# Performance work log

Measured on AMD Instinct MI355X. Metric: run time of the kernel, lower is better.

## Reference

```python
import jax, jax.numpy as jnp
import numpy as np

# --- model dims (from init_kwargs + Mamba3 args) ---
D_MODEL = 256            # hidden_dim
D_INNER = 2 * D_MODEL    # expand=2
D_STATE = 8
HEADDIM = 16
NHEADS = D_INNER // HEADDIM  # 32
CHUNK = 8
D_CONV = 4
CONV_DIM = D_INNER + 2 * D_STATE            # x,B,C share the depthwise conv
D_INPROJ = 2 * D_INNER + 2 * D_STATE + NHEADS  # z,xBC,dt
INPUT_DIM = 57
OUT_SIZE = 6
BATCH = 16
SEQLEN = 4096


def setup_inputs() -> dict:
    key = jax.random.key(0)
    ks = jax.random.split(key, 12)
    def w(k, shape, s=0.02):
        return jax.random.normal(k, shape, dtype=jnp.float32) * s
    # dt bias initialized so softplus(dt_bias) ~ [1e-3, 1e-1] (Mamba-style)
    dt0 = jnp.exp(jax.random.uniform(ks[4], (NHEADS,), minval=jnp.log(1e-3), maxval=jnp.log(1e-1)))
    dt_bias = dt0 + jnp.log(-jnp.expm1(-dt0))  # inverse softplus
    return {
        "x": jax.random.normal(ks[0], (BATCH, SEQLEN, INPUT_DIM), dtype=jnp.float32),
        "W_in": w(ks[1], (D_MODEL, INPUT_DIM)),
        "b_in": jnp.zeros((D_MODEL,), jnp.float32),
        "W_inproj": w(ks[2], (D_INPROJ, D_MODEL)),
        "conv_w": w(ks[3], (CONV_DIM, D_CONV), 0.2),
        "conv_b": jnp.zeros((CONV_DIM,), jnp.float32),
        "dt_bias": dt_bias.astype(jnp.float32),
        "A_log": jnp.log(jax.random.uniform(ks[5], (NHEADS,), minval=1.0, maxval=16.0)).astype(jnp.float32),
        "D": jnp.ones((NHEADS,), jnp.float32),
        "W_out": w(ks[6], (D_MODEL, D_INNER)),
        "W_cls": w(ks[7], (OUT_SIZE, D_MODEL)),
        "b_cls": jnp.zeros((OUT_SIZE,), jnp.float32),
    }


def reference(x, W_in, b_in, W_inproj, conv_w, conv_b, dt_bias, A_log, D, W_out, W_cls, b_cls):
    Bsz, Lq, _ = x.shape
    h = x @ W_in.T + b_in                                  # [B,L,D_MODEL]
    zxbcdt = h @ W_inproj.T                                # [B,L,D_INPROJ]
    z = zxbcdt[..., :D_INNER]
    xBC = zxbcdt[..., D_INNER:D_INNER + CONV_DIM]
    dt = zxbcdt[..., -NHEADS:]
    # causal depthwise conv1d (kernel D_CONV) + SiLU
    xp = jnp.pad(xBC, ((0, 0), (D_CONV - 1, 0), (0, 0)))
    conv = sum(xp[:, k:k + Lq, :] * conv_w[:, k] for k in range(D_CONV)) + conv_b
    xBC = jax.nn.silu(conv)
    xs = xBC[..., :D_INNER]
    Bm = xBC[..., D_INNER:D_INNER + D_STATE]               # [B,L,N]
    Cm = xBC[..., -D_STATE:]                               # [B,L,N]
    dt = jax.nn.softplus(dt + dt_bias)                     # [B,L,H]
    A = -jnp.exp(A_log)                                    # [H]
    # --- chunked SSD selective scan (SISO: scalar A per head) ---
    Nc = Lq // CHUNK
    xh = xs.reshape(Bsz, Nc, CHUNK, NHEADS, HEADDIM)
    Bc = Bm.reshape(Bsz, Nc, CHUNK, D_STATE)
    Cc = Cm.reshape(Bsz, Nc, CHUNK, D_STATE)
    dtc = dt.reshape(Bsz, Nc, CHUNK, NHEADS)
    cA = jnp.cumsum(dtc * A, axis=2)                       # [B,Nc,cs,H]
    # intra-chunk: y_i += sum_{j<=i} (C_i.B_j) exp(cA_i-cA_j) dt_j x_j
    Lmat = jnp.exp(cA[:, :, :, None, :] - cA[:, :, None, :, :])   # [B,Nc,i,j,H]
    mask = jnp.tril(jnp.ones((CHUNK, CHUNK), bool))
    Lmat = jnp.where(mask[None, None, :, :, None], Lmat, 0.0)
    CB = jnp.einsum('bcin,bcjn->bcij', Cc, Bc)
    scores = CB[..., None] * Lmat * dtc[:, :, None, :, :]
    y_intra = jnp.einsum('bcijh,bcjhp->bcihp', scores, xh)
    # per-chunk end states and decays
    dec_end = jnp.exp(cA[:, :, -1:, :] - cA)               # [B,Nc,cs,H]
    S = jnp.einsum('bcjh,bcjn,bcjhp->bchpn', dec_end * dtc, Bc, xh)
    chunk_dec = jnp.exp(cA[:, :, -1, :])                   # [B,Nc,H]
    def step(hc, inp):
        Sc, dc = inp
        return hc * dc[:, :, None, None] + Sc, hc          # emit state BEFORE chunk
    h0 = jnp.zeros((Bsz, NHEADS, HEADDIM, D_STATE), x.dtype)
    _, hprev = jax.lax.scan(step, h0, (jnp.moveaxis(S, 1, 0), jnp.moveaxis(chunk_dec, 1, 0)))
    hprev = jnp.moveaxis(hprev, 0, 1)                      # [B,Nc,H,P,N]
    y_inter = jnp.einsum('bchpn,bcin,bcih->bcihp', hprev, Cc, jnp.exp(cA))
    y = y_intra + y_inter + D[None, None, None, :, None] * xh
    y = y.reshape(Bsz, Lq, D_INNER)
    y = y * jax.nn.silu(z)                                 # z gate (no out-proj norm)
    out = y @ W_out.T                                      # [B,L,D_MODEL]
    pooled = out.mean(axis=1)                              # AdaptiveAvgPool1d(1)
    return pooled @ W_cls.T + b_cls                        # [B,OUT_SIZE]
```

## Files before the change

kernel.cpp:

```cpp
#include <hip/hip_runtime.h>
#include <math.h>

#define BATCH 16
#define SEQLEN 4096
#define INPUT_DIM 57
#define D_MODEL 256
#define D_INNER 512
#define D_STATE 8
#define HEADDIM 16
#define NHEADS 32
#define CHUNK 8
#define NC (SEQLEN/CHUNK)
#define NCH (NC/2)
#define CONV_DIM 528
#define D_INPROJ 1072
#define OUT_SIZE 6
#define NTOK (BATCH*SEQLEN)
#define NSEG 16
#define SEGC (NCH/NSEG)

__device__ __forceinline__ unsigned short f2bf(float f) {
    unsigned v = __float_as_uint(f);
    return (unsigned short)((v + 0x7fffu + ((v >> 16) & 1u)) >> 16);
}
__device__ __forceinline__ unsigned pack_bf2(float lo, float hi) {
    unsigned r;
    asm("v_cvt_pk_bf16_f32 %0, %1, %2" : "=v"(r) : "v"(lo), "v"(hi));
    return r;
}
__device__ __forceinline__ float fsilu(float v) {
    return v * __builtin_amdgcn_rcpf(1.f + __expf(-v));
}

typedef __attribute__((ext_vector_type(8))) short bf16x8;
typedef __attribute__((ext_vector_type(4))) float f32x4;

__global__ __launch_bounds__(256) void precompute_kernel(
    const float* __restrict__ W_in,
    const float* __restrict__ b_in,
    const float* __restrict__ W_inproj,
    const float* __restrict__ W_out,
    const float* __restrict__ W_cls,
    float* __restrict__ WcT,
    float* __restrict__ b_comb,
    unsigned short* __restrict__ Wbf,
    float* __restrict__ W_oc)
{
    __shared__ double red[256];
    const int blk = blockIdx.x;
    const int tid = threadIdx.x;
    if (blk < D_INPROJ) {
        const int n = blk;
        const int t = tid & 63, ms = tid >> 6;
        double a0 = 0.0, a1 = 0.0;
        const int m0 = ms*64;
        if (t < INPUT_DIM) {
            for (int m = m0; m < m0 + 64; m += 2) {
                a0 += (double)W_inproj[n*D_MODEL+m  ] * (double)W_in[(m  )*INPUT_DIM+t];
                a1 += (double)W_inproj[n*D_MODEL+m+1] * (double)W_in[(m+1)*INPUT_DIM+t];
            }
        } else if (t == INPUT_DIM) {
            for (int m = m0; m < m0 + 64; m += 2) {
                a0 += (double)W_inproj[n*D_MODEL+m  ] * (double)b_in[m  ];
                a1 += (double)W_inproj[n*D_MODEL+m+1] * (double)b_in[m+1];
            }
        }
        red[tid] = a0 + a1;
        __syncthreads();
        if (tid < 64) {
            double acc = (red[tid] + red[tid+64]) + (red[tid+128] + red[tid+192]);
            if (t < INPUT_DIM) {
                WcT[t*D_INPROJ + n] = (float)acc;
                if (n < 1024) Wbf[n*64 + t] = f2bf((float)acc);
            } else {
                if (t == INPUT_DIM) b_comb[n] = (float)acc;
                if (n < 1024) Wbf[n*64 + t] = 0;
            }
        }
    } else {
        const int d = blk - D_INPROJ;
        const int o = tid >> 5;
        const int lp = tid & 31;
        double a = 0.0;
        if (o < OUT_SIZE) {
            const int m0 = lp*8;
            #pragma unroll
            for (int mm = 0; mm < 8; ++mm) {
                int m = m0 + mm;
                a += (double)W_cls[o*D_MODEL+m] * (double)W_out[m*D_INNER+d];
            }
        }
        #pragma unroll
        for (int off = 16; off > 0; off >>= 1)
            a += __shfl_down(a, off, 32);
        if (o < OUT_SIZE && lp == 0)
            W_oc[o*D_INNER + d] = (float)a;
    }
}

#define XS(r,k)       uni[(r)*68 + (k)]
#define EX(r,c)       uni[2176 + (r)*48 + (c)]
#define ELS2(cw,h,i)  uni[3088 + (((cw)*32+(h))*8) + (i)]
#define GCO2(cw,h,j)  uni[3600 + (((cw)*32+(h))*8) + (j)]
#define SCL3(cw,h,o)  uni[(((cw)*32+(h))*48) + (o)]

__global__ __launch_bounds__(256) void fused_kernel(
    const float* __restrict__ x,
    const unsigned short* __restrict__ Wbf,
    const float* __restrict__ WcT,
    const float* __restrict__ bcomb,
    const float* __restrict__ conv_w,
    const float* __restrict__ conv_b,
    const float* __restrict__ dt_bias,
    const float* __restrict__ A_log,
    const float* __restrict__ Dvec,
    unsigned* __restrict__ SGg,
    float* __restrict__ cdec,
    float* __restrict__ partial_intra)
{
    __shared__ __attribute__((aligned(16))) float uni[4112];
    __shared__ __attribute__((aligned(16))) float Bs[2][8][12], Cs[2][8][12];
    __shared__ float dts[2][8][33], cAl[2][8][33];
    __shared__ float CBl[2][8][8];

    const int blk = blockIdx.x;
    const int b = blk >> 8, cp = blk & 255;
    const int scBase = (b << 8) + cp;
    const int tid = threadIdx.x;
    const long t0 = (long)b*SEQLEN + (long)cp*16;
    const bool first = (cp == 0);

    #pragma unroll
    for (int it = 0; it < 8; ++it) {
        int idx = tid + it*256;
        int r = idx >> 6, k = idx & 63;
        float v = 0.f;
        if (k < INPUT_DIM && (r >= 16 || !first))
            v = x[(t0 - 16 + r)*INPUT_DIM + k];
        XS(r, k) = v;
    }
    __syncthreads();

    const int lane = tid & 63, wv = tid >> 6;
    const int quad = lane >> 4, mrow = lane & 15;

    bf16x8 aM[2], aH[2];
    #pragma unroll
    for (int hf = 0; hf < 2; ++hf) {
        const float* sm = &XS(16 + mrow, hf*32 + quad*8);
        const float* sh = &XS(mrow,      hf*32 + quad*8);
        unsigned* pm = (unsigned*)&aM[hf];
        unsigned* ph = (unsigned*)&aH[hf];
        #pragma unroll
        for (int j = 0; j < 4; ++j) {
            pm[j] = pack_bf2(sm[2*j], sm[2*j+1]);
            ph[j] = pack_bf2(sh[2*j], sh[2*j+1]);
        }
    }

    if (tid < 192) {
        const int col = tid % 48;
        const int grp = tid / 48;
        const int r0 = grp*5;
        const int nr = (grp == 3) ? 4 : 5;
        const float be = bcomb[1024 + col];
        float a[5];
        #pragma unroll
        for (int j = 0; j < 5; ++j) a[j] = be;
        for (int k = 0; k < INPUT_DIM; ++k) {
            const float w = WcT[(size_t)k*D_INPROJ + 1024 + col];
            #pragma unroll
            for (int j = 0; j < 5; ++j)
                if (j < nr) a[j] += w*XS(13 + r0 + j, k);
        }
        #pragma unroll
        for (int j = 0; j < 5; ++j) {
            if (j < nr) {
                int r = r0 + j;
                EX(r, col) = (first && r < 3) ? 0.f : a[j];
            }
        }
    }
    __syncthreads();

    if (tid < 32) {
        const int cw = tid >> 4, q = tid & 15;
        const int ch = 512 + q;
        const float4 cw4 = *(const float4*)&conv_w[ch*4];
        const float cb = conv_b[ch];
        float s0 = EX(cw*8+0, q), s1 = EX(cw*8+1, q), s2 = EX(cw*8+2, q);
        #pragma unroll
        for (int i = 0; i < 8; ++i) {
            float s3 = EX(cw*8+i+3, q);
            float v = cb + s0*cw4.x + s1*cw4.y + s2*cw4.z + s3*cw4.w;
            v = fsilu(v);
            if (q < 8) Bs[cw][i][q] = v; else Cs[cw][i][q-8] = v;
            s0 = s1; s1 = s2; s2 = s3;
        }
    } else if (tid >= 64 && tid < 128) {
        const int cw = (tid - 64) >> 5, h = (tid - 64) & 31;
        const float Ah = -__expf(A_log[h]);
        const float db = dt_bias[h];
        float ca = 0.f;
        #pragma unroll
        for (int i = 0; i < 8; ++i) {
            float raw = EX(cw*8 + i + 3, 16 + h) + db;
            float dt = (raw > 20.f) ? raw : log1pf(__expf(raw));
            dts[cw][i][h] = dt;
            ca += dt * Ah;
            cAl[cw][i][h] = ca;
            ELS2(cw, h, i) = __expf(ca);
        }
    }
    __syncthreads();

    if (tid < 128) {
        const int cw = tid >> 6, i = (tid >> 3) & 7, j = tid & 7;
        float s = 0.f;
        #pragma unroll
        for (int n = 0; n < 8; ++n) s += Cs[cw][i][n]*Bs[cw][j][n];
        CBl[cw][i][j] = s;
    } else if (tid < 160) {
        const int h = tid - 128;
        cdec[(size_t)scBase*32 + h] = ELS2(0, h, 7) * ELS2(1, h, 7);
    }
    __syncthreads();

    #pragma unroll
    for (int q = 0; q < 12; ++q) {
        int idx = tid + q*256;
        int ofs = idx % 48;
        int hc  = idx / 48;
        int h2 = hc & 31, cw2 = hc >> 5;
        int i, j;
        if (ofs < 16) { i = ofs >> 2; j = ofs & 3; }
        else { int r2 = ofs - 16; i = 4 + (r2 >> 3); j = r2 & 7; }
        float v = 0.f;
        if (j <= i)
            v = CBl[cw2][i][j]
              * __expf(cAl[cw2][i][h2] - cAl[cw2][j][h2]) * dts[cw2][j][h2];
        SCL3(cw2, h2, ofs) = v;
    }
    #pragma unroll
    for (int q = 0; q < 2; ++q) {
        int idx = tid + q*256;
        int j = idx & 7; int hc = idx >> 3;
        int h2 = hc & 31, cw2 = hc >> 5;
        GCO2(cw2, h2, j) = __expf(cAl[cw2][7][h2] - cAl[cw2][j][h2]) * dts[cw2][j][h2];
    }
    __syncthreads();

    const int cw   = quad >> 1;
    const int joff = (quad & 1) * 4;
    const int srcConv = (lane + 48) & 63;
    const float zm = (quad & 1) ? 0.f : 1.f;

    #pragma unroll
    for (int t = 0; t < 8; ++t) {
        const int g   = wv + 4*t;
        const int h   = g;
        const int col = g*16 + mrow;

        const unsigned short* wpz = &Wbf[(size_t)col*64];
        bf16x8 bz0 = *(const bf16x8*)&wpz[quad*8];
        bf16x8 bz1 = *(const bf16x8*)&wpz[32 + quad*8];
        const float bvz = bcomb[col];
        f32x4 accZ; accZ.x = bvz; accZ.y = bvz; accZ.z = bvz; accZ.w = bvz;
        accZ = __builtin_amdgcn_mfma_f32_16x16x32_bf16(aM[0], bz0, accZ, 0, 0, 0);
        accZ = __builtin_amdgcn_mfma_f32_16x16x32_bf16(aM[1], bz1, accZ, 0, 0, 0);

        const unsigned short* wpx = &Wbf[(size_t)(col + 512)*64];
        bf16x8 bx0 = *(const bf16x8*)&wpx[quad*8];
        bf16x8 bx1 = *(const bf16x8*)&wpx[32 + quad*8];
        const float bvx = bcomb[col + 512];
        f32x4 accXM; accXM.x = bvx; accXM.y = bvx; accXM.z = bvx; accXM.w = bvx;
        accXM = __builtin_amdgcn_mfma_f32_16x16x32_bf16(aM[0], bx0, accXM, 0, 0, 0);
        accXM = __builtin_amdgcn_mfma_f32_16x16x32_bf16(aM[1], bx1, accXM, 0, 0, 0);
        f32x4 accXH; accXH.x = bvx; accXH.y = bvx; accXH.z = bvx; accXH.w = bvx;
        accXH = __builtin_amdgcn_mfma_f32_16x16x32_bf16(aH[0], bx0, accXH, 0, 0, 0);
        accXH = __builtin_amdgcn_mfma_f32_16x16x32_bf16(aH[1], bx1, accXH, 0, 0, 0);

        float s1 = (quad == 3) ? accXH[3] : accXM[3];
        float s2 = (quad == 3) ? accXH[2] : accXM[2];
        float s3 = (quad == 3) ? accXH[1] : accXM[1];
        float r1 = __shfl(s1, srcConv, 64);
        float r2 = __shfl(s2, srcConv, 64);
        float r3 = __shfl(s3, srcConv, 64);
        if (first && quad == 0) { r1 = 0.f; r2 = 0.f; r3 = 0.f; }

        const float4 cw4 = *(const float4*)&conv_w[col*4];
        const float cb = conv_b[col];
        float vals[7] = {r3, r2, r1, accXM[0], accXM[1], accXM[2], accXM[3]};
        float xv[4], szv[4];
        #pragma unroll
        for (int r = 0; r < 4; ++r) {
            float v = cb + vals[r]*cw4.x + vals[r+1]*cw4.y + vals[r+2]*cw4.z + vals[r+3]*cw4.w;
            xv[r] = fsilu(v);
            szv[r] = fsilu(accZ[r]);
        }

        const float* sbase = &SCL3(cw, h, 0);
        float part[8];
        #pragma unroll
        for (int i = 0; i < 4; ++i) {
            f32x4 c4 = *(const f32x4*)&sbase[i*4];
            part[i] = zm*(c4[0]*xv[0] + c4[1]*xv[1] + c4[2]*xv[2] + c4[3]*xv[3]);
        }
        #pragma unroll
        for (int i = 4; i < 8; ++i) {
            f32x4 c4 = *(const f32x4*)&sbase[16 + (i-4)*8 + joff];
            part[i] = c4[0]*xv[0] + c4[1]*xv[1] + c4[2]*xv[2] + c4[3]*xv[3];
        }

        const float Dv = Dvec[h];
        float pa = 0.f;
        #pragma unroll
        for (int r = 0; r < 4; ++r) {
            float mine   = (quad & 1) ? part[4+r] : part[r];
            float theirs = (quad & 1) ? part[r]   : part[4+r];
            float other  = __shfl_xor(theirs, 16, 64);
            float y = Dv*xv[r] + mine + other;
            pa += y * szv[r];
        }
        pa += __shfl_xor(pa, 16, 64);
        float paO = __shfl_xor(pa, 32, 64);

        f32x4 G4 = *(const f32x4*)&GCO2(cw, h, joff);
        f32x4 E4 = *(const f32x4*)&ELS2(cw, h, joff);
        float sn[8], gg[8];
        #pragma unroll
        for (int n = 0; n < 8; ++n) { sn[n] = 0.f; gg[n] = 0.f; }
        #pragma unroll
        for (int r = 0; r < 4; ++r) {
            const int il = joff + r;
            float w  = szv[r]*E4[r];
            float uu = G4[r]*xv[r];
            const float4 B0 = *(const float4*)&Bs[cw][il][0];
            const float4 B1 = *(const float4*)&Bs[cw][il][4];
            const float4 C0 = *(const float4*)&Cs[cw][il][0];
            const float4 C1 = *(const float4*)&Cs[cw][il][4];
            sn[0] += uu*B0.x; sn[1] += uu*B0.y; sn[2] += uu*B0.z; sn[3] += uu*B0.w;
            sn[4] += uu*B1.x; sn[5] += uu*B1.y; sn[6] += uu*B1.z; sn[7] += uu*B1.w;
            gg[0] += w*C0.x;  gg[1] += w*C0.y;  gg[2] += w*C0.z;  gg[3] += w*C0.w;
            gg[4] += w*C1.x;  gg[5] += w*C1.y;  gg[6] += w*C1.z;  gg[7] += w*C1.w;
        }
        float sC[8], gC[8];
        #pragma unroll
        for (int n = 0; n < 8; ++n) {
            unsigned pk = pack_bf2(sn[n], gg[n]);
            unsigned pv = (unsigned)__shfl_xor((int)pk, 16, 64);
            sC[n] = sn[n] + __uint_as_float(pv << 16);
            gC[n] = gg[n] + __uint_as_float(pv & 0xffff0000u);
        }
        const float d0 = ELS2(0, h, 7), d1 = ELS2(1, h, 7);
        float local = 0.f;
        unsigned up[8];
        #pragma unroll
        for (int n = 0; n < 8; ++n) {
            unsigned pk = pack_bf2(sC[n], gC[n]);
            unsigned pv = (unsigned)__shfl_xor((int)pk, 32, 64);
            float So = __uint_as_float(pv << 16);
            float go = __uint_as_float(pv & 0xffff0000u);
            float Sp = sC[n]*d1 + So;
            float Gp = gC[n] + d0*go;
            local += sC[n]*go;
            up[n] = pack_bf2(Sp, Gp);
        }
        if (quad == 0) {
            partial_intra[(size_t)scBase*512 + col] = pa + paO + local;
            unsigned* dst = &SGg[((size_t)scBase*32 + h)*128 + mrow*8];
            *(uint4*)&dst[0] = *(uint4*)&up[0];
            *(uint4*)&dst[4] = *(uint4*)&up[4];
        }
    }
}

__global__ __launch_bounds__(128) void scanseg_kernel(
    const unsigned* __restrict__ SGg,
    const float* __restrict__ cdec,
    float* __restrict__ Sloc,
    float* __restrict__ Gseg,
    float* __restrict__ Aseg,
    float* __restrict__ ploc)
{
    const int blk = blockIdx.x;
    const int seg = blk & (NSEG-1);
    const int bh  = blk >> 4;
    const int b = bh >> 5, h = bh & 31;
    const int tid = threadIdx.x;
    const int c0 = seg*SEGC;

    float s = 0.f, P = 1.f, G = 0.f, pooled = 0.f;
    const unsigned* src = &SGg[((size_t)(b*NCH + c0)*32 + h)*128 + tid];
    const float* dsrc = &cdec[(b*NCH + c0)*32 + h];

    #pragma unroll 4
    for (int cc = 0; cc < SEGC; ++cc) {
        unsigned u = src[(size_t)cc*4096];
        float d = dsrc[cc*32];
        float Sv = __uint_as_float(u << 16);
        float gv = __uint_as_float(u & 0xffff0000u);
        pooled += s * gv;
        G += P * gv;
        P *= d;
        s = s*d + Sv;
    }
    Sloc[(size_t)blk*128 + tid] = s;
    Gseg[(size_t)blk*128 + tid] = G;
    if (tid == 0) Aseg[blk] = P;

    float t = pooled;
    t += __shfl_down(t, 4, 8);
    t += __shfl_down(t, 2, 8);
    t += __shfl_down(t, 1, 8);
    if ((tid & 7) == 0) ploc[(size_t)blk*16 + (tid >> 3)] = t;
}

__global__ __launch_bounds__(128) void scancomb_kernel(
    const float* __restrict__ Sloc,
    const float* __restrict__ Gseg,
    const float* __restrict__ Aseg,
    const float* __restrict__ ploc,
    double* __restrict__ partial_inter)
{
    __shared__ double red[128];
    const int bh = blockIdx.x;
    const int tid = threadIdx.x;
    float s = 0.f;
    double acc = 0.0;
    for (int seg = 0; seg < NSEG; ++seg) {
        size_t base = (size_t)(bh*NSEG + seg);
        float Gv = Gseg[base*128 + tid];
        float Av = Aseg[base];
        float Sv = Sloc[base*128 + tid];
        acc += (double)(s * Gv);
        s = s*Av + Sv;
    }
    red[tid] = acc;
    __syncthreads();
    if (tid < 16) {
        double t = 0.0;
        #pragma unroll
        for (int n = 0; n < 8; ++n) t += red[tid*8 + n];
        for (int seg = 0; seg < NSEG; ++seg)
            t += (double)ploc[(size_t)(bh*NSEG + seg)*16 + tid];
        partial_inter[(size_t)bh*16 + tid] = t;
    }
}

__global__ __launch_bounds__(256) void reduce_intra_kernel(
    const float* __restrict__ pIn,
    float* __restrict__ pred)
{
    const int g = blockIdx.x & 31;
    const int b = blockIdx.x >> 5;
    const int tid = threadIdx.x;
    for (int col = tid; col < 512; col += 256) {
        float s = 0.f;
        #pragma unroll 4
        for (int c = 0; c < 8; ++c)
            s += pIn[((size_t)b*NCH + g*8 + c)*512 + col];
        pred[((size_t)(b*32) + g)*512 + col] = s;
    }
}

__global__ __launch_bounds__(512) void final_kernel(
    const float* __restrict__ pred,
    const double* __restrict__ partial_inter,
    const float* __restrict__ W_oc,
    const float* __restrict__ b_cls,
    float* __restrict__ out)
{
    __shared__ double pooled[512];
    const int b = blockIdx.x, tid = threadIdx.x;
    double ssum = 0.0;
    for (int g = 0; g < 32; ++g)
        ssum += (double)pred[((size_t)(b*32) + g)*512 + tid];
    ssum += partial_inter[(size_t)b*512 + tid];
    pooled[tid] = ssum * (1.0/(double)SEQLEN);
    __syncthreads();
    if (tid < OUT_SIZE*64) {
        const int o = tid >> 6, l = tid & 63;
        double acc = 0.0;
        for (int m = l; m < 512; m += 64)
            acc += pooled[m] * (double)W_oc[o*512 + m];
        #pragma unroll
        for (int off = 32; off > 0; off >>= 1)
            acc += __shfl_down(acc, off);
        if (l == 0) out[b*OUT_SIZE + o] = (float)(acc + (double)b_cls[o]);
    }
}

extern "C" void kernel_launch(void* const* d_in, const int* in_sizes, int n_in,
                              void* d_out, int out_size, void* d_ws, size_t ws_size,
                              hipStream_t stream)
{
    const float* x        = (const float*)d_in[0];
    const float* W_in     = (const float*)d_in[1];
    const float* b_in     = (const float*)d_in[2];
    const float* W_inproj = (const float*)d_in[3];
    const float* conv_w   = (const float*)d_in[4];
    const float* conv_b   = (const float*)d_in[5];
    const float* dt_bias  = (const float*)d_in[6];
    const float* A_log    = (const float*)d_in[7];
    const float* Dvec     = (const float*)d_in[8];
    const float* W_out    = (const float*)d_in[9];
    const float* W_cls    = (const float*)d_in[10];
    const float* b_cls    = (const float*)d_in[11];
    float* out = (float*)d_out;

    char* ws = (char*)d_ws;
    size_t off = 0;
    auto alloc = [&](size_t bytes) -> void* {
        void* p = ws + off;
        off += (bytes + 255) & ~(size_t)255;
        return p;
    };
    unsigned* SGg = (unsigned*)alloc((size_t)BATCH*NCH*32*128*4);
    float*  cdecb = (float*) alloc((size_t)BATCH*NCH*32*4);
    float*  pIn   = (float*) alloc((size_t)BATCH*NCH*512*4);
    float*  SlocB = (float*) alloc((size_t)BATCH*NHEADS*NSEG*128*4);
    float*  GsegB = (float*) alloc((size_t)BATCH*NHEADS*NSEG*128*4);
    float*  AsegB = (float*) alloc((size_t)BATCH*NHEADS*NSEG*4);
    float*  plocB = (float*) alloc((size_t)BATCH*NHEADS*NSEG*16*4);
    float*  pred  = (float*) alloc((size_t)BATCH*32*512*4);
    double* pIt   = (double*)alloc((size_t)BATCH*512*8);
    float*  WcT   = (float*) alloc((size_t)INPUT_DIM*D_INPROJ*4);
    float*  bcomb = (float*) alloc((size_t)D_INPROJ*4);
    unsigned short* Wbf = (unsigned short*)alloc((size_t)1024*64*2);
    float*  Woc   = (float*) alloc((size_t)OUT_SIZE*D_INNER*4);
    if (off > ws_size) return;

    precompute_kernel<<<D_INPROJ + D_INNER, 256, 0, stream>>>(W_in, b_in, W_inproj, W_out, W_cls,
                                                              WcT, bcomb, Wbf, Woc);
    fused_kernel<<<BATCH*NC/2, 256, 0, stream>>>(x, Wbf, WcT, bcomb, conv_w, conv_b,
                                                 dt_bias, A_log, Dvec, SGg, cdecb, pIn);
    scanseg_kernel<<<BATCH*NHEADS*NSEG, 128, 0, stream>>>(SGg, cdecb, SlocB, GsegB, AsegB, plocB);
    scancomb_kernel<<<BATCH*NHEADS, 128, 0, stream>>>(SlocB, GsegB, AsegB, plocB, pIt);
    reduce_intra_kernel<<<BATCH*32, 256, 0, stream>>>(pIn, pred);
    final_kernel<<<BATCH, 512, 0, stream>>>(pred, pIt, Woc, b_cls, out);
}
```

Measured before the change: 293.2 us.

## Fuse intra-chunk reduction into fused kernel via atomics and consolidate shared memory

Removes the reduce_intra kernel and its pIn buffer: the fused kernel now atomically adds each per-chunk-pair partial sum straight into pred, which the precompute kernel zeroes beforehand. Shared memory is packed into one union array, B and C are merged into a single array, and the cumulative-A array is dropped. The exp of differences is replaced by a ratio of stored exponentials. This saves one launch and a global round trip, at the cost of atomic contention and some risk to accuracy from dividing exponentials.

```diff
diff --git a/kernel.cpp b/kernel.cpp
--- a/kernel.cpp
+++ b/kernel.cpp
@@ -44,7 +44,8 @@
     float* __restrict__ WcT,
     float* __restrict__ b_comb,
     unsigned short* __restrict__ Wbf,
-    float* __restrict__ W_oc)
+    float* __restrict__ W_oc,
+    float* __restrict__ pred)
 {
     __shared__ double red[256];
     const int blk = blockIdx.x;
@@ -79,6 +80,9 @@
         }
     } else {
         const int d = blk - D_INPROJ;
+        const int zi = d*256 + tid;
+        pred[zi] = 0.f;
+        pred[zi + 131072] = 0.f;
         const int o = tid >> 5;
         const int lp = tid & 31;
         double a = 0.0;
@@ -100,9 +104,11 @@
 
 #define XS(r,k)       uni[(r)*68 + (k)]
 #define EX(r,c)       uni[2176 + (r)*48 + (c)]
-#define ELS2(cw,h,i)  uni[3088 + (((cw)*32+(h))*8) + (i)]
-#define GCO2(cw,h,j)  uni[3600 + (((cw)*32+(h))*8) + (j)]
 #define SCL3(cw,h,o)  uni[(((cw)*32+(h))*48) + (o)]
+#define DTS(cw,i,h)   uni[3088 + ((cw)*8+(i))*33 + (h)]
+#define ELS2(cw,h,i)  uni[3616 + (((cw)*32+(h))*8) + (i)]
+#define GCO2(cw,h,j)  uni[4128 + (((cw)*32+(h))*8) + (j)]
+#define CBL(cw,i,j)   uni[4640 + (cw)*64 + (i)*8 + (j)]
 
 __global__ __launch_bounds__(256) void fused_kernel(
     const float* __restrict__ x,
@@ -116,12 +122,10 @@
     const float* __restrict__ Dvec,
     unsigned* __restrict__ SGg,
     float* __restrict__ cdec,
-    float* __restrict__ partial_intra)
+    float* __restrict__ pred)
 {
-    __shared__ __attribute__((aligned(16))) float uni[4112];
-    __shared__ __attribute__((aligned(16))) float Bs[2][8][12], Cs[2][8][12];
-    __shared__ float dts[2][8][33], cAl[2][8][33];
-    __shared__ float CBl[2][8][8];
+    __shared__ __attribute__((aligned(16))) float uni[4768];
+    __shared__ __attribute__((aligned(16))) float BC[2][8][20];
 
     const int blk = blockIdx.x;
     const int b = blk >> 8, cp = blk & 255;
@@ -194,7 +198,7 @@
             float s3 = EX(cw*8+i+3, q);
             float v = cb + s0*cw4.x + s1*cw4.y + s2*cw4.z + s3*cw4.w;
             v = fsilu(v);
-            if (q < 8) Bs[cw][i][q] = v; else Cs[cw][i][q-8] = v;
+            BC[cw][i][q] = v;
             s0 = s1; s1 = s2; s2 = s3;
         }
     } else if (tid >= 64 && tid < 128) {
@@ -206,9 +210,8 @@
         for (int i = 0; i < 8; ++i) {
             float raw = EX(cw*8 + i + 3, 16 + h) + db;
             float dt = (raw > 20.f) ? raw : log1pf(__expf(raw));
-            dts[cw][i][h] = dt;
+            DTS(cw, i, h) = dt;
             ca += dt * Ah;
-            cAl[cw][i][h] = ca;
             ELS2(cw, h, i) = __expf(ca);
         }
     }
@@ -218,8 +221,8 @@
         const int cw = tid >> 6, i = (tid >> 3) & 7, j = tid & 7;
         float s = 0.f;
         #pragma unroll
-        for (int n = 0; n < 8; ++n) s += Cs[cw][i][n]*Bs[cw][j][n];
-        CBl[cw][i][j] = s;
+        for (int n = 0; n < 8; ++n) s += BC[cw][i][8+n]*BC[cw][j][n];
+        CBL(cw, i, j) = s;
     } else if (tid < 160) {
         const int h = tid - 128;
         cdec[(size_t)scBase*32 + h] = ELS2(0, h, 7) * ELS2(1, h, 7);
@@ -237,8 +240,8 @@
         else { int r2 = ofs - 16; i = 4 + (r2 >> 3); j = r2 & 7; }
         float v = 0.f;
         if (j <= i)
-            v = CBl[cw2][i][j]
-              * __expf(cAl[cw2][i][h2] - cAl[cw2][j][h2]) * dts[cw2][j][h2];
+            v = CBL(cw2, i, j)
+              * (ELS2(cw2, h2, i) / ELS2(cw2, h2, j)) * DTS(cw2, j, h2);
         SCL3(cw2, h2, ofs) = v;
     }
     #pragma unroll
@@ -246,7 +249,7 @@
         int idx = tid + q*256;
         int j = idx & 7; int hc = idx >> 3;
         int h2 = hc & 31, cw2 = hc >> 5;
-        GCO2(cw2, h2, j) = __expf(cAl[cw2][7][h2] - cAl[cw2][j][h2]) * dts[cw2][j][h2];
+        GCO2(cw2, h2, j) = (ELS2(cw2, h2, 7) / ELS2(cw2, h2, j)) * DTS(cw2, j, h2);
     }
     __syncthreads();
 
@@ -335,10 +338,10 @@
             const int il = joff + r;
             float w  = szv[r]*E4[r];
             float uu = G4[r]*xv[r];
-            const float4 B0 = *(const float4*)&Bs[cw][il][0];
-            const float4 B1 = *(const float4*)&Bs[cw][il][4];
-            const float4 C0 = *(const float4*)&Cs[cw][il][0];
-            const float4 C1 = *(const float4*)&Cs[cw][il][4];
+            const float4 B0 = *(const float4*)&BC[cw][il][0];
+            const float4 B1 = *(const float4*)&BC[cw][il][4];
+            const float4 C0 = *(const float4*)&BC[cw][il][8];
+            const float4 C1 = *(const float4*)&BC[cw][il][12];
             sn[0] += uu*B0.x; sn[1] += uu*B0.y; sn[2] += uu*B0.z; sn[3] += uu*B0.w;
             sn[4] += uu*B1.x; sn[5] += uu*B1.y; sn[6] += uu*B1.z; sn[7] += uu*B1.w;
             gg[0] += w*C0.x;  gg[1] += w*C0.y;  gg[2] += w*C0.z;  gg[3] += w*C0.w;
@@ -367,7 +370,7 @@
             up[n] = pack_bf2(Sp, Gp);
         }
         if (quad == 0) {
-            partial_intra[(size_t)scBase*512 + col] = pa + paO + local;
+            atomicAdd(&pred[((size_t)(b*32) + (cp >> 3))*512 + col], pa + paO + local);
             unsigned* dst = &SGg[((size_t)scBase*32 + h)*128 + mrow*8];
             *(uint4*)&dst[0] = *(uint4*)&up[0];
             *(uint4*)&dst[4] = *(uint4*)&up[4];
@@ -448,22 +451,6 @@
     }
 }
 
-__global__ __launch_bounds__(256) void reduce_intra_kernel(
-    const float* __restrict__ pIn,
-    float* __restrict__ pred)
-{
-    const int g = blockIdx.x & 31;
-    const int b = blockIdx.x >> 5;
-    const int tid = threadIdx.x;
-    for (int col = tid; col < 512; col += 256) {
-        float s = 0.f;
-        #pragma unroll 4
-        for (int c = 0; c < 8; ++c)
-            s += pIn[((size_t)b*NCH + g*8 + c)*512 + col];
-        pred[((size_t)(b*32) + g)*512 + col] = s;
-    }
-}
-
 __global__ __launch_bounds__(512) void final_kernel(
     const float* __restrict__ pred,
     const double* __restrict__ partial_inter,
@@ -518,7 +505,6 @@
     };
     unsigned* SGg = (unsigned*)alloc((size_t)BATCH*NCH*32*128*4);
     float*  cdecb = (float*) alloc((size_t)BATCH*NCH*32*4);
-    float*  pIn   = (float*) alloc((size_t)BATCH*NCH*512*4);
     float*  SlocB = (float*) alloc((size_t)BATCH*NHEADS*NSEG*128*4);
     float*  GsegB = (float*) alloc((size_t)BATCH*NHEADS*NSEG*128*4);
     float*  AsegB = (float*) alloc((size_t)BATCH*NHEADS*NSEG*4);
@@ -532,11 +518,10 @@
     if (off > ws_size) return;
 
     precompute_kernel<<<D_INPROJ + D_INNER, 256, 0, stream>>>(W_in, b_in, W_inproj, W_out, W_cls,
-                                                              WcT, bcomb, Wbf, Woc);
+                                                              WcT, bcomb, Wbf, Woc, pred);
     fused_kernel<<<BATCH*NC/2, 256, 0, stream>>>(x, Wbf, WcT, bcomb, conv_w, conv_b,
-                                                 dt_bias, A_log, Dvec, SGg, cdecb, pIn);
+                                                 dt_bias, A_log, Dvec, SGg, cdecb, pred);
     scanseg_kernel<<<BATCH*NHEADS*NSEG, 128, 0, stream>>>(SGg, cdecb, SlocB, GsegB, AsegB, plocB);
     scancomb_kernel<<<BATCH*NHEADS, 128, 0, stream>>>(SlocB, GsegB, AsegB, plocB, pIt);
-    reduce_intra_kernel<<<BATCH*32, 256, 0, stream>>>(pIn, pred);
     final_kernel<<<BATCH, 512, 0, stream>>>(pred, pIt, Woc, b_cls, out);
 }
```

After: 277.4 us. 1.06x faster.
